# Kernel optimization log

Measured on AMD Instinct MI355X. Metric: run time of the kernel, lower is better.

Reference implementation:

```python
import jax, jax.numpy as jnp
import numpy as np

N_NODES = 50000
N_EDGES = 1600000
IN_DIM = 1024
MID_DIM = 256


def setup_inputs() -> dict:
    key = jax.random.key(0)
    k1, k2, k3, k4 = jax.random.split(key, 4)
    x = jax.random.normal(k1, (N_NODES, IN_DIM), dtype=jnp.float32)
    edge_index = jax.random.randint(k2, (2, N_EDGES), 0, N_NODES, dtype=jnp.int64)
    # Glorot-style init like PyG GCNConv
    W1 = jax.random.normal(k3, (IN_DIM, MID_DIM), dtype=jnp.float32) * (2.0 / (IN_DIM + MID_DIM)) ** 0.5
    W2 = jax.random.normal(k4, (MID_DIM, IN_DIM), dtype=jnp.float32) * (2.0 / (MID_DIM + IN_DIM)) ** 0.5
    b1 = jnp.zeros((MID_DIM,), dtype=jnp.float32)
    b2 = jnp.zeros((IN_DIM,), dtype=jnp.float32)
    return {"x": x, "edge_index": edge_index, "W1": W1, "b1": b1, "W2": W2, "b2": b2}


def _gcn_conv(x, W, b, src, dst, norm, n):
    # PyG GCNConv: linear transform first, then normalized neighbor sum, then bias.
    xw = x @ W                                   # [N, F_out]
    msg = xw[src] * norm[:, None]                # gather + scale, [E+N, F_out]
    out = jax.ops.segment_sum(msg, dst, num_segments=n)
    return out + b


def reference(x, edge_index, W1, b1, W2, b2):
    n = x.shape[0]
    loops = jnp.arange(n, dtype=edge_index.dtype)
    src = jnp.concatenate([edge_index[0], loops])
    dst = jnp.concatenate([edge_index[1], loops])
    # symmetric normalization with self-loops: D^-1/2 (A+I) D^-1/2
    deg = jax.ops.segment_sum(jnp.ones_like(dst, dtype=x.dtype), dst, num_segments=n)
    dis = jnp.where(deg > 0, jax.lax.rsqrt(jnp.maximum(deg, 1.0)), 0.0)
    norm = dis[src] * dis[dst]                   # [E+N]
    h = jax.nn.relu(_gcn_conv(x, W1, b1, src, dst, norm, n))
    # F.dropout(training=False) is identity at inference
    out = _gcn_conv(h, W2, b2, src, dst, norm, n)
    return out
```

## Files before the change

### kernel.cpp

```cpp
#include <hip/hip_runtime.h>

typedef unsigned short u16;
typedef u16 u16x8 __attribute__((ext_vector_type(8)));
typedef u16 u16x4 __attribute__((ext_vector_type(4)));
typedef short s16x8 __attribute__((ext_vector_type(8)));
typedef float f32x4 __attribute__((ext_vector_type(4)));

__device__ __forceinline__ float b2f(u16 u) {
  unsigned int v = ((unsigned int)u) << 16;
  return __builtin_bit_cast(float, v);
}
__device__ __forceinline__ u16 f2b(float f) {
  unsigned int u = __builtin_bit_cast(unsigned int, f);
  u += 0x7FFFu + ((u >> 16) & 1u);
  return (u16)(u >> 16);
}

__global__ void deg_kernel(const int* __restrict__ dst, int* __restrict__ deg, int E, int n) {
  int e = blockIdx.x * 256 + threadIdx.x;
  if (e < E) {
    int d = dst[e];
    d = min(max(d, 0), n - 1);
    atomicAdd(&deg[d], 1);
  }
}

__global__ void dis_kernel(const int* __restrict__ deg, float* __restrict__ dis, int n) {
  int i = blockIdx.x * 256 + threadIdx.x;
  if (i < n) dis[i] = 1.0f / sqrtf((float)(deg[i] + 1));
}

__global__ __launch_bounds__(256) void scanA(const int* __restrict__ cnt, int* __restrict__ bsum, int n) {
  __shared__ int s[256];
  int t = threadIdx.x, i = blockIdx.x * 256 + t;
  s[t] = (i < n) ? cnt[i] : 0;
  __syncthreads();
  for (int off = 128; off > 0; off >>= 1) {
    if (t < off) s[t] += s[t + off];
    __syncthreads();
  }
  if (t == 0) bsum[blockIdx.x] = s[0];
}

__global__ __launch_bounds__(256) void scanB(int* __restrict__ bsum, int nb) {
  __shared__ int s[256];
  int t = threadIdx.x;
  int v = (t < nb) ? bsum[t] : 0;
  s[t] = v;
  __syncthreads();
  for (int off = 1; off < 256; off <<= 1) {
    int x = (t >= off) ? s[t - off] : 0;
    __syncthreads();
    s[t] += x;
    __syncthreads();
  }
  if (t < nb) bsum[t] = s[t] - v;
}

__global__ __launch_bounds__(256) void scanC(const int* __restrict__ cnt, const int* __restrict__ bsum,
                                             int* __restrict__ rowp, int n) {
  __shared__ int s[256];
  int t = threadIdx.x, i = blockIdx.x * 256 + t;
  int v = (i < n) ? cnt[i] : 0;
  s[t] = v;
  __syncthreads();
  for (int off = 1; off < 256; off <<= 1) {
    int x = (t >= off) ? s[t - off] : 0;
    __syncthreads();
    s[t] += x;
    __syncthreads();
  }
  if (i < n) rowp[i + 1] = bsum[blockIdx.x] + s[t];
  if (i == 0) rowp[0] = 0;
}

__global__ void fill_kernel(const int* __restrict__ src, const int* __restrict__ dst,
                            const int* __restrict__ rowp, int* __restrict__ fill,
                            const float* __restrict__ dis, int* __restrict__ csr_s,
                            float* __restrict__ csr_w, int E, int n) {
  int e = blockIdx.x * 256 + threadIdx.x;
  if (e < E) {
    int s = src[e]; s = min(max(s, 0), n - 1);
    int d = dst[e]; d = min(max(d, 0), n - 1);
    int pos = rowp[d] + atomicAdd(&fill[d], 1);
    csr_s[pos] = s;
    csr_w[pos] = dis[s] * dis[d];
  }
}

__global__ void transpose_cvt(const float* __restrict__ in, u16* __restrict__ out, int K, int N) {
  int idx = blockIdx.x * 256 + threadIdx.x;
  if (idx < K * N) {
    int k = idx / N, nn = idx - k * N;
    out[(size_t)nn * K + k] = f2b(in[idx]);
  }
}

template <bool A_F32, bool OUT_F32>
__global__ __launch_bounds__(256) void gemm_kernel(const void* __restrict__ Ap,
                                                   const u16* __restrict__ BT,
                                                   const float* __restrict__ bias,
                                                   void* __restrict__ Cp, int M, int N, int K) {
  __shared__ u16 As[128 * 40];
  __shared__ u16 Bs[128 * 40];
  const int tid = threadIdx.x;
  const int m0 = blockIdx.y * 128, n0 = blockIdx.x * 128;
  const int lane = tid & 63, wv = tid >> 6;
  const int wr = (wv >> 1) * 64, wc = (wv & 1) * 64;
  const int q = lane >> 4, l = lane & 15;
  f32x4 acc[4][4] = {};

  for (int kt = 0; kt < K; kt += 32) {
    if (A_F32) {
      const float* A = (const float*)Ap;
#pragma unroll
      for (int i = 0; i < 4; i++) {
        int t = tid + i * 256;
        int r = t >> 3, k4 = (t & 7) * 4;
        float4 av = make_float4(0.f, 0.f, 0.f, 0.f);
        int gr = m0 + r;
        if (gr < M) av = *(const float4*)&A[(size_t)gr * K + kt + k4];
        u16x4 o;
        o[0] = f2b(av.x); o[1] = f2b(av.y); o[2] = f2b(av.z); o[3] = f2b(av.w);
        *(u16x4*)&As[r * 40 + k4] = o;
      }
    } else {
      const u16* A = (const u16*)Ap;
#pragma unroll
      for (int i = 0; i < 2; i++) {
        int t = tid + i * 256;
        int r = t >> 2, k8 = (t & 3) * 8;
        u16x8 av = {};
        int gr = m0 + r;
        if (gr < M) av = *(const u16x8*)&A[(size_t)gr * K + kt + k8];
        *(u16x8*)&As[r * 40 + k8] = av;
      }
    }
#pragma unroll
    for (int i = 0; i < 2; i++) {
      int t = tid + i * 256;
      int r = t >> 2, k8 = (t & 3) * 8;
      *(u16x8*)&Bs[r * 40 + k8] = *(const u16x8*)&BT[(size_t)(n0 + r) * K + kt + k8];
    }
    __syncthreads();
    s16x8 af[4], bf[4];
#pragma unroll
    for (int mi = 0; mi < 4; mi++) af[mi] = *(const s16x8*)&As[(wr + mi * 16 + l) * 40 + q * 8];
#pragma unroll
    for (int ni = 0; ni < 4; ni++) bf[ni] = *(const s16x8*)&Bs[(wc + ni * 16 + l) * 40 + q * 8];
#pragma unroll
    for (int mi = 0; mi < 4; mi++)
#pragma unroll
      for (int ni = 0; ni < 4; ni++)
        acc[mi][ni] = __builtin_amdgcn_mfma_f32_16x16x32_bf16(af[mi], bf[ni], acc[mi][ni], 0, 0, 0);
    __syncthreads();
  }

#pragma unroll
  for (int ni = 0; ni < 4; ni++) {
    int col = n0 + wc + ni * 16 + l;
    float bv = bias ? bias[col] : 0.f;
#pragma unroll
    for (int mi = 0; mi < 4; mi++) {
#pragma unroll
      for (int j = 0; j < 4; j++) {
        int row = m0 + wr + mi * 16 + q * 4 + j;
        if (row < M) {
          float v = acc[mi][ni][j] + bv;
          if (OUT_F32)
            ((float*)Cp)[(size_t)row * N + col] = v;
          else
            ((u16*)Cp)[(size_t)row * N + col] = f2b(v);
        }
      }
    }
  }
}

template <bool RELU>
__global__ __launch_bounds__(256) void agg_kernel(const u16* __restrict__ tab,
                                                  const int* __restrict__ rowp,
                                                  const int* __restrict__ csr_s,
                                                  const float* __restrict__ csr_w,
                                                  const float* __restrict__ dis,
                                                  const float* __restrict__ bias,
                                                  u16* __restrict__ out, int n) {
  int wv = threadIdx.x >> 6, lane = threadIdx.x & 63;
  int node = blockIdx.x * 4 + wv;
  if (node >= n) return;
  int f0 = lane * 4;
  float sw = dis[node];
  sw *= sw;
  u16x4 v = *(const u16x4*)&tab[(size_t)node * 256 + f0];
  float a0 = sw * b2f(v[0]), a1 = sw * b2f(v[1]), a2 = sw * b2f(v[2]), a3 = sw * b2f(v[3]);
  int e0 = rowp[node], e1 = rowp[node + 1];
  for (int e = e0; e < e1; e++) {
    int s = csr_s[e];
    float w = csr_w[e];
    u16x4 u = *(const u16x4*)&tab[(size_t)s * 256 + f0];
    a0 += w * b2f(u[0]);
    a1 += w * b2f(u[1]);
    a2 += w * b2f(u[2]);
    a3 += w * b2f(u[3]);
  }
  if (RELU) {
    a0 = fmaxf(a0 + bias[f0 + 0], 0.f);
    a1 = fmaxf(a1 + bias[f0 + 1], 0.f);
    a2 = fmaxf(a2 + bias[f0 + 2], 0.f);
    a3 = fmaxf(a3 + bias[f0 + 3], 0.f);
  }
  u16x4 o;
  o[0] = f2b(a0); o[1] = f2b(a1); o[2] = f2b(a2); o[3] = f2b(a3);
  *(u16x4*)&out[(size_t)node * 256 + f0] = o;
}

extern "C" void kernel_launch(void* const* d_in, const int* in_sizes, int n_in,
                              void* d_out, int out_size, void* d_ws, size_t ws_size,
                              hipStream_t stream) {
  const float* x  = (const float*)d_in[0];
  const int*   ei = (const int*)d_in[1];
  const float* W1 = (const float*)d_in[2];
  const float* b1 = (const float*)d_in[3];
  const float* W2 = (const float*)d_in[4];
  const float* b2 = (const float*)d_in[5];

  const int MID = in_sizes[3];
  const int IN  = in_sizes[5];
  const int n   = in_sizes[0] / IN;
  const int E   = in_sizes[1] / 2;
  const int* srcv = ei;
  const int* dstv = ei + E;

  char* w = (char*)d_ws;
  size_t off = 0;
  auto alloc = [&](size_t bytes) -> void* {
    void* p = w + off;
    off += (bytes + 255) & ~(size_t)255;
    return p;
  };
  int*   deg   = (int*)alloc((size_t)n * 4);
  int*   rowp  = (int*)alloc((size_t)(n + 1) * 4);
  int*   fill  = (int*)alloc((size_t)n * 4);
  int*   bsum  = (int*)alloc(1024);
  int*   csr_s = (int*)alloc((size_t)E * 4);
  float* csr_w = (float*)alloc((size_t)E * 4);
  float* dis   = (float*)alloc((size_t)n * 4);
  u16*   W1T   = (u16*)alloc((size_t)IN * MID * 2);
  u16*   W2T   = (u16*)alloc((size_t)IN * MID * 2);
  u16*   xw    = (u16*)alloc((size_t)n * MID * 2);
  u16*   h     = (u16*)alloc((size_t)n * MID * 2);
  u16*   ah    = xw;

  hipMemsetAsync(deg, 0, (size_t)n * 4, stream);
  hipMemsetAsync(fill, 0, (size_t)n * 4, stream);

  transpose_cvt<<<(IN * MID + 255) / 256, 256, 0, stream>>>(W1, W1T, IN, MID);
  transpose_cvt<<<(IN * MID + 255) / 256, 256, 0, stream>>>(W2, W2T, MID, IN);

  const int nb = (n + 255) / 256;
  deg_kernel<<<(E + 255) / 256, 256, 0, stream>>>(dstv, deg, E, n);
  dis_kernel<<<nb, 256, 0, stream>>>(deg, dis, n);
  scanA<<<nb, 256, 0, stream>>>(deg, bsum, n);
  scanB<<<1, 256, 0, stream>>>(bsum, nb);
  scanC<<<nb, 256, 0, stream>>>(deg, bsum, rowp, n);
  fill_kernel<<<(E + 255) / 256, 256, 0, stream>>>(srcv, dstv, rowp, fill, dis, csr_s, csr_w, E, n);

  dim3 g1(MID / 128, (n + 127) / 128);
  gemm_kernel<true, false><<<g1, 256, 0, stream>>>(x, W1T, nullptr, xw, n, MID, IN);
  agg_kernel<true><<<(n + 3) / 4, 256, 0, stream>>>(xw, rowp, csr_s, csr_w, dis, b1, h, n);
  agg_kernel<false><<<(n + 3) / 4, 256, 0, stream>>>(h, rowp, csr_s, csr_w, dis, nullptr, ah, n);
  dim3 g2(IN / 128, (n + 127) / 128);
  gemm_kernel<false, true><<<g2, 256, 0, stream>>>(ah, W2T, b2, d_out, n, IN, MID);
}
```

Measured before the change: 1.080 ms.

## Double-buffer GEMM LDS tiles and unroll edge gather loop by four

The GEMM kernel now uses two LDS buffers. It prefetches the next K-tile into registers while MFMAs run on the current tile, then stores it to the alternate buffer, so only one barrier is needed per iteration. This hides global-load latency, at the cost of double LDS use and more registers, which may lower occupancy. The aggregation kernel also unrolls its neighbor loop by four so several independent gathers are in flight at once. This changes the float summation order slightly.

```diff
diff --git a/kernel.cpp b/kernel.cpp
--- a/kernel.cpp
+++ b/kernel.cpp
@@ -101,8 +101,8 @@
                                                    const u16* __restrict__ BT,
                                                    const float* __restrict__ bias,
                                                    void* __restrict__ Cp, int M, int N, int K) {
-  __shared__ u16 As[128 * 40];
-  __shared__ u16 Bs[128 * 40];
+  __shared__ u16 As[2][128 * 40];
+  __shared__ u16 Bs[2][128 * 40];
   const int tid = threadIdx.x;
   const int m0 = blockIdx.y * 128, n0 = blockIdx.x * 128;
   const int lane = tid & 63, wv = tid >> 6;
@@ -110,19 +110,20 @@
   const int q = lane >> 4, l = lane & 15;
   f32x4 acc[4][4] = {};
 
-  for (int kt = 0; kt < K; kt += 32) {
+  float4 aregf[4];
+  u16x8 aregb[2];
+  u16x8 breg[2];
+
+  auto load_tile = [&](int kt) {
     if (A_F32) {
       const float* A = (const float*)Ap;
 #pragma unroll
       for (int i = 0; i < 4; i++) {
         int t = tid + i * 256;
         int r = t >> 3, k4 = (t & 7) * 4;
-        float4 av = make_float4(0.f, 0.f, 0.f, 0.f);
         int gr = m0 + r;
-        if (gr < M) av = *(const float4*)&A[(size_t)gr * K + kt + k4];
-        u16x4 o;
-        o[0] = f2b(av.x); o[1] = f2b(av.y); o[2] = f2b(av.z); o[3] = f2b(av.w);
-        *(u16x4*)&As[r * 40 + k4] = o;
+        aregf[i] = make_float4(0.f, 0.f, 0.f, 0.f);
+        if (gr < M) aregf[i] = *(const float4*)&A[(size_t)gr * K + kt + k4];
       }
     } else {
       const u16* A = (const u16*)Ap;
@@ -130,30 +131,69 @@
       for (int i = 0; i < 2; i++) {
         int t = tid + i * 256;
         int r = t >> 2, k8 = (t & 3) * 8;
-        u16x8 av = {};
         int gr = m0 + r;
-        if (gr < M) av = *(const u16x8*)&A[(size_t)gr * K + kt + k8];
-        *(u16x8*)&As[r * 40 + k8] = av;
+        aregb[i] = (u16x8){};
+        if (gr < M) aregb[i] = *(const u16x8*)&A[(size_t)gr * K + kt + k8];
       }
     }
 #pragma unroll
     for (int i = 0; i < 2; i++) {
       int t = tid + i * 256;
       int r = t >> 2, k8 = (t & 3) * 8;
-      *(u16x8*)&Bs[r * 40 + k8] = *(const u16x8*)&BT[(size_t)(n0 + r) * K + kt + k8];
-    }
-    __syncthreads();
+      breg[i] = *(const u16x8*)&BT[(size_t)(n0 + r) * K + kt + k8];
+    }
+  };
+
+  auto store_tile = [&](int buf) {
+    if (A_F32) {
+#pragma unroll
+      for (int i = 0; i < 4; i++) {
+        int t = tid + i * 256;
+        int r = t >> 3, k4 = (t & 7) * 4;
+        u16x4 o;
+        o[0] = f2b(aregf[i].x); o[1] = f2b(aregf[i].y);
+        o[2] = f2b(aregf[i].z); o[3] = f2b(aregf[i].w);
+        *(u16x4*)&As[buf][r * 40 + k4] = o;
+      }
+    } else {
+#pragma unroll
+      for (int i = 0; i < 2; i++) {
+        int t = tid + i * 256;
+        int r = t >> 2, k8 = (t & 3) * 8;
+        *(u16x8*)&As[buf][r * 40 + k8] = aregb[i];
+      }
+    }
+#pragma unroll
+    for (int i = 0; i < 2; i++) {
+      int t = tid + i * 256;
+      int r = t >> 2, k8 = (t & 3) * 8;
+      *(u16x8*)&Bs[buf][r * 40 + k8] = breg[i];
+    }
+  };
+
+  load_tile(0);
+  store_tile(0);
+  __syncthreads();
+
+  int cur = 0;
+  for (int kt = 0; kt < K; kt += 32) {
+    const bool has_next = (kt + 32) < K;
+    if (has_next) load_tile(kt + 32);
+
     s16x8 af[4], bf[4];
 #pragma unroll
-    for (int mi = 0; mi < 4; mi++) af[mi] = *(const s16x8*)&As[(wr + mi * 16 + l) * 40 + q * 8];
-#pragma unroll
-    for (int ni = 0; ni < 4; ni++) bf[ni] = *(const s16x8*)&Bs[(wc + ni * 16 + l) * 40 + q * 8];
+    for (int mi = 0; mi < 4; mi++) af[mi] = *(const s16x8*)&As[cur][(wr + mi * 16 + l) * 40 + q * 8];
+#pragma unroll
+    for (int ni = 0; ni < 4; ni++) bf[ni] = *(const s16x8*)&Bs[cur][(wc + ni * 16 + l) * 40 + q * 8];
 #pragma unroll
     for (int mi = 0; mi < 4; mi++)
 #pragma unroll
       for (int ni = 0; ni < 4; ni++)
         acc[mi][ni] = __builtin_amdgcn_mfma_f32_16x16x32_bf16(af[mi], bf[ni], acc[mi][ni], 0, 0, 0);
-    __syncthreads();
+
+    if (has_next) store_tile(cur ^ 1);
+    __syncthreads();
+    cur ^= 1;
   }
 
 #pragma unroll
@@ -194,7 +234,20 @@
   u16x4 v = *(const u16x4*)&tab[(size_t)node * 256 + f0];
   float a0 = sw * b2f(v[0]), a1 = sw * b2f(v[1]), a2 = sw * b2f(v[2]), a3 = sw * b2f(v[3]);
   int e0 = rowp[node], e1 = rowp[node + 1];
-  for (int e = e0; e < e1; e++) {
+  int e = e0;
+  for (; e + 4 <= e1; e += 4) {
+    int s0 = csr_s[e], s1 = csr_s[e + 1], s2 = csr_s[e + 2], s3 = csr_s[e + 3];
+    float w0 = csr_w[e], w1 = csr_w[e + 1], w2 = csr_w[e + 2], w3 = csr_w[e + 3];
+    u16x4 u0 = *(const u16x4*)&tab[(size_t)s0 * 256 + f0];
+    u16x4 u1 = *(const u16x4*)&tab[(size_t)s1 * 256 + f0];
+    u16x4 u2 = *(const u16x4*)&tab[(size_t)s2 * 256 + f0];
+    u16x4 u3 = *(const u16x4*)&tab[(size_t)s3 * 256 + f0];
+    a0 += w0 * b2f(u0[0]) + w1 * b2f(u1[0]) + w2 * b2f(u2[0]) + w3 * b2f(u3[0]);
+    a1 += w0 * b2f(u0[1]) + w1 * b2f(u1[1]) + w2 * b2f(u2[1]) + w3 * b2f(u3[1]);
+    a2 += w0 * b2f(u0[2]) + w1 * b2f(u1[2]) + w2 * b2f(u2[2]) + w3 * b2f(u3[2]);
+    a3 += w0 * b2f(u0[3]) + w1 * b2f(u1[3]) + w2 * b2f(u2[3]) + w3 * b2f(u3[3]);
+  }
+  for (; e < e1; e++) {
     int s = csr_s[e];
     float w = csr_w[e];
     u16x4 u = *(const u16x4*)&tab[(size_t)s * 256 + f0];
```

After: 878.6 us. 1.23x faster.

## Replace LDS-tiled GEMM with register-streamed double-buffered MFMA; unroll aggregation by four

Applied to the files above, without the earlier changes.

The GEMM drops shared memory and barriers. Each wave loads its A and B fragments straight from global memory into registers, double-buffered across k-steps so loads overlap MFMA work, and converts f32 to bf16 with packed cvt instructions. Tiles change to 64 rows by 256 columns per block, with each wave owning 64 columns. The aggregation loop is unrolled by four edges to keep more gathers in flight. The risks are that A and B data shared between waves is no longer reused through LDS, raising global and L2 traffic, and that register pressure grows.

```diff
diff --git a/kernel.cpp b/kernel.cpp
--- a/kernel.cpp
+++ b/kernel.cpp
@@ -97,74 +97,101 @@
 }
 
 template <bool A_F32, bool OUT_F32>
-__global__ __launch_bounds__(256) void gemm_kernel(const void* __restrict__ Ap,
+__global__ __launch_bounds__(256) void gemm_stream(const void* __restrict__ Ap,
                                                    const u16* __restrict__ BT,
                                                    const float* __restrict__ bias,
                                                    void* __restrict__ Cp, int M, int N, int K) {
-  __shared__ u16 As[128 * 40];
-  __shared__ u16 Bs[128 * 40];
   const int tid = threadIdx.x;
-  const int m0 = blockIdx.y * 128, n0 = blockIdx.x * 128;
-  const int lane = tid & 63, wv = tid >> 6;
-  const int wr = (wv >> 1) * 64, wc = (wv & 1) * 64;
-  const int q = lane >> 4, l = lane & 15;
+  const int lane = tid & 63;
+  const int wv = tid >> 6;
+  const int l = lane & 15, q = lane >> 4;
+  const int m0 = blockIdx.y * 64;
+  const int n0 = blockIdx.x * 256 + wv * 64;
+
+  const float* afp[4];
+  const u16*   abp[4];
+  const u16*   bbp[4];
+#pragma unroll
+  for (int mi = 0; mi < 4; mi++) {
+    int r = m0 + mi * 16 + l;
+    if (r > M - 1) r = M - 1;
+    if (A_F32) afp[mi] = (const float*)Ap + (size_t)r * K + q * 8;
+    else       abp[mi] = (const u16*)Ap + (size_t)r * K + q * 8;
+  }
+#pragma unroll
+  for (int ni = 0; ni < 4; ni++) {
+    int c = n0 + ni * 16 + l;
+    bbp[ni] = BT + (size_t)c * K + q * 8;
+  }
+
   f32x4 acc[4][4] = {};
-
-  for (int kt = 0; kt < K; kt += 32) {
+  float4 arA[4][2], arB[4][2];
+  u16x8 abA[4], abB[4];
+  u16x8 brA[4], brB[4];
+  s16x8 af[4];
+
+  auto loadA = [&](float4 (&ar)[4][2], u16x8 (&ab)[4], int kt) {
     if (A_F32) {
-      const float* A = (const float*)Ap;
-#pragma unroll
-      for (int i = 0; i < 4; i++) {
-        int t = tid + i * 256;
-        int r = t >> 3, k4 = (t & 7) * 4;
-        float4 av = make_float4(0.f, 0.f, 0.f, 0.f);
-        int gr = m0 + r;
-        if (gr < M) av = *(const float4*)&A[(size_t)gr * K + kt + k4];
-        u16x4 o;
-        o[0] = f2b(av.x); o[1] = f2b(av.y); o[2] = f2b(av.z); o[3] = f2b(av.w);
-        *(u16x4*)&As[r * 40 + k4] = o;
+#pragma unroll
+      for (int mi = 0; mi < 4; mi++) {
+        ar[mi][0] = *(const float4*)(afp[mi] + kt);
+        ar[mi][1] = *(const float4*)(afp[mi] + kt + 4);
       }
     } else {
-      const u16* A = (const u16*)Ap;
-#pragma unroll
-      for (int i = 0; i < 2; i++) {
-        int t = tid + i * 256;
-        int r = t >> 2, k8 = (t & 3) * 8;
-        u16x8 av = {};
-        int gr = m0 + r;
-        if (gr < M) av = *(const u16x8*)&A[(size_t)gr * K + kt + k8];
-        *(u16x8*)&As[r * 40 + k8] = av;
+#pragma unroll
+      for (int mi = 0; mi < 4; mi++) ab[mi] = *(const u16x8*)(abp[mi] + kt);
+    }
+  };
+  auto loadB = [&](u16x8 (&br)[4], int kt) {
+#pragma unroll
+    for (int ni = 0; ni < 4; ni++) br[ni] = *(const u16x8*)(bbp[ni] + kt);
+  };
+  auto cvtA = [&](float4 (&ar)[4][2], u16x8 (&ab)[4]) {
+    if (A_F32) {
+#pragma unroll
+      for (int mi = 0; mi < 4; mi++) {
+        unsigned int d0, d1, d2, d3;
+        asm("v_cvt_pk_bf16_f32 %0, %1, %2" : "=v"(d0) : "v"(ar[mi][0].x), "v"(ar[mi][0].y));
+        asm("v_cvt_pk_bf16_f32 %0, %1, %2" : "=v"(d1) : "v"(ar[mi][0].z), "v"(ar[mi][0].w));
+        asm("v_cvt_pk_bf16_f32 %0, %1, %2" : "=v"(d2) : "v"(ar[mi][1].x), "v"(ar[mi][1].y));
+        asm("v_cvt_pk_bf16_f32 %0, %1, %2" : "=v"(d3) : "v"(ar[mi][1].z), "v"(ar[mi][1].w));
+        int4 di; di.x = d0; di.y = d1; di.z = d2; di.w = d3;
+        af[mi] = __builtin_bit_cast(s16x8, di);
       }
+    } else {
+#pragma unroll
+      for (int mi = 0; mi < 4; mi++) af[mi] = __builtin_bit_cast(s16x8, ab[mi]);
     }
-#pragma unroll
-    for (int i = 0; i < 2; i++) {
-      int t = tid + i * 256;
-      int r = t >> 2, k8 = (t & 3) * 8;
-      *(u16x8*)&Bs[r * 40 + k8] = *(const u16x8*)&BT[(size_t)(n0 + r) * K + kt + k8];
-    }
-    __syncthreads();
-    s16x8 af[4], bf[4];
-#pragma unroll
-    for (int mi = 0; mi < 4; mi++) af[mi] = *(const s16x8*)&As[(wr + mi * 16 + l) * 40 + q * 8];
-#pragma unroll
-    for (int ni = 0; ni < 4; ni++) bf[ni] = *(const s16x8*)&Bs[(wc + ni * 16 + l) * 40 + q * 8];
+  };
+  auto domfma = [&](u16x8 (&br)[4]) {
 #pragma unroll
     for (int mi = 0; mi < 4; mi++)
 #pragma unroll
       for (int ni = 0; ni < 4; ni++)
-        acc[mi][ni] = __builtin_amdgcn_mfma_f32_16x16x32_bf16(af[mi], bf[ni], acc[mi][ni], 0, 0, 0);
-    __syncthreads();
+        acc[mi][ni] = __builtin_amdgcn_mfma_f32_16x16x32_bf16(
+            af[mi], __builtin_bit_cast(s16x8, br[ni]), acc[mi][ni], 0, 0, 0);
+  };
+
+  loadA(arA, abA, 0);
+  loadB(brA, 0);
+  for (int kt = 0; kt < K; kt += 64) {
+    if (kt + 32 < K) { loadA(arB, abB, kt + 32); loadB(brB, kt + 32); }
+    cvtA(arA, abA);
+    domfma(brA);
+    if (kt + 64 < K) { loadA(arA, abA, kt + 64); loadB(brA, kt + 64); }
+    cvtA(arB, abB);
+    domfma(brB);
   }
 
 #pragma unroll
   for (int ni = 0; ni < 4; ni++) {
-    int col = n0 + wc + ni * 16 + l;
+    int col = n0 + ni * 16 + l;
     float bv = bias ? bias[col] : 0.f;
 #pragma unroll
     for (int mi = 0; mi < 4; mi++) {
 #pragma unroll
       for (int j = 0; j < 4; j++) {
-        int row = m0 + wr + mi * 16 + q * 4 + j;
+        int row = m0 + mi * 16 + q * 4 + j;
         if (row < M) {
           float v = acc[mi][ni][j] + bv;
           if (OUT_F32)
@@ -194,7 +221,20 @@
   u16x4 v = *(const u16x4*)&tab[(size_t)node * 256 + f0];
   float a0 = sw * b2f(v[0]), a1 = sw * b2f(v[1]), a2 = sw * b2f(v[2]), a3 = sw * b2f(v[3]);
   int e0 = rowp[node], e1 = rowp[node + 1];
-  for (int e = e0; e < e1; e++) {
+  int e = e0;
+  for (; e + 4 <= e1; e += 4) {
+    int s0 = csr_s[e], s1 = csr_s[e + 1], s2 = csr_s[e + 2], s3 = csr_s[e + 3];
+    float w0 = csr_w[e], w1 = csr_w[e + 1], w2 = csr_w[e + 2], w3 = csr_w[e + 3];
+    u16x4 u0 = *(const u16x4*)&tab[(size_t)s0 * 256 + f0];
+    u16x4 u1 = *(const u16x4*)&tab[(size_t)s1 * 256 + f0];
+    u16x4 u2 = *(const u16x4*)&tab[(size_t)s2 * 256 + f0];
+    u16x4 u3 = *(const u16x4*)&tab[(size_t)s3 * 256 + f0];
+    a0 += w0 * b2f(u0[0]) + w1 * b2f(u1[0]) + w2 * b2f(u2[0]) + w3 * b2f(u3[0]);
+    a1 += w0 * b2f(u0[1]) + w1 * b2f(u1[1]) + w2 * b2f(u2[1]) + w3 * b2f(u3[1]);
+    a2 += w0 * b2f(u0[2]) + w1 * b2f(u1[2]) + w2 * b2f(u2[2]) + w3 * b2f(u3[2]);
+    a3 += w0 * b2f(u0[3]) + w1 * b2f(u1[3]) + w2 * b2f(u2[3]) + w3 * b2f(u3[3]);
+  }
+  for (; e < e1; e++) {
     int s = csr_s[e];
     float w = csr_w[e];
     u16x4 u = *(const u16x4*)&tab[(size_t)s * 256 + f0];
@@ -265,10 +305,10 @@
   scanC<<<nb, 256, 0, stream>>>(deg, bsum, rowp, n);
   fill_kernel<<<(E + 255) / 256, 256, 0, stream>>>(srcv, dstv, rowp, fill, dis, csr_s, csr_w, E, n);
 
-  dim3 g1(MID / 128, (n + 127) / 128);
-  gemm_kernel<true, false><<<g1, 256, 0, stream>>>(x, W1T, nullptr, xw, n, MID, IN);
+  dim3 g1(MID / 256, (n + 63) / 64);
+  gemm_stream<true, false><<<g1, 256, 0, stream>>>(x, W1T, nullptr, xw, n, MID, IN);
   agg_kernel<true><<<(n + 3) / 4, 256, 0, stream>>>(xw, rowp, csr_s, csr_w, dis, b1, h, n);
   agg_kernel<false><<<(n + 3) / 4, 256, 0, stream>>>(h, rowp, csr_s, csr_w, dis, nullptr, ah, n);
-  dim3 g2(IN / 128, (n + 127) / 128);
-  gemm_kernel<false, true><<<g2, 256, 0, stream>>>(ah, W2T, b2, d_out, n, IN, MID);
-}
+  dim3 g2(IN / 256, (n + 63) / 64);
+  gemm_stream<false, true><<<g2, 256, 0, stream>>>(ah, W2T, b2, d_out, n, IN, MID);
+}
```

Measured after the change: 974.3 us. 1.11x faster.

## Use direct global-to-LDS loads with XOR swizzle in GEMM; unroll aggregation gathers

Applied to the files above, without the earlier changes.

The GEMM tile loads now use global_load_lds to copy 16-byte chunks straight into LDS, with an XOR-swizzled layout instead of padded rows. For the fp32 input, the bf16 conversion moves to after the LDS read using v_cvt_pk_bf16_f32, so LDS holds fp32 and is twice as large. The aggregation loop is unrolled by four so several neighbour gathers are in flight at once. Together these aim to cut register staging and VGPR round trips in the loads and to raise memory-level parallelism in the gather. The out-of-range rows are now clamped rather than zeroed.

```diff
diff --git a/kernel.cpp b/kernel.cpp
--- a/kernel.cpp
+++ b/kernel.cpp
@@ -14,6 +14,12 @@
   unsigned int u = __builtin_bit_cast(unsigned int, f);
   u += 0x7FFFu + ((u >> 16) & 1u);
   return (u16)(u >> 16);
+}
+
+__device__ __forceinline__ void gld16(void* lds, const void* g) {
+  __builtin_amdgcn_global_load_lds(
+      (const __attribute__((address_space(1))) void*)g,
+      (__attribute__((address_space(3))) void*)lds, 16, 0, 0);
 }
 
 __global__ void deg_kernel(const int* __restrict__ dst, int* __restrict__ deg, int E, int n) {
@@ -97,12 +103,15 @@
 }
 
 template <bool A_F32, bool OUT_F32>
-__global__ __launch_bounds__(256) void gemm_kernel(const void* __restrict__ Ap,
-                                                   const u16* __restrict__ BT,
-                                                   const float* __restrict__ bias,
-                                                   void* __restrict__ Cp, int M, int N, int K) {
-  __shared__ u16 As[128 * 40];
-  __shared__ u16 Bs[128 * 40];
+__global__ __launch_bounds__(256) void gemm_m97(const void* __restrict__ Ap,
+                                                const u16* __restrict__ BT,
+                                                const float* __restrict__ bias,
+                                                void* __restrict__ Cp, int M, int N, int K) {
+  constexpr int ABYTES = A_F32 ? 16384 : 8192;
+  __shared__ alignas(16) unsigned char smem[ABYTES + 8192];
+  unsigned char* Asm = smem;
+  unsigned char* Bsm = smem + ABYTES;
+
   const int tid = threadIdx.x;
   const int m0 = blockIdx.y * 128, n0 = blockIdx.x * 128;
   const int lane = tid & 63, wv = tid >> 6;
@@ -110,44 +119,76 @@
   const int q = lane >> 4, l = lane & 15;
   f32x4 acc[4][4] = {};
 
+  constexpr int NA = A_F32 ? 4 : 2;
+  constexpr size_t AB = A_F32 ? 4 : 2;
+  const char* a_src[NA];
+  const char* b_src[2];
+#pragma unroll
+  for (int i = 0; i < NA; i++) {
+    int c = tid + i * 256;
+    int r, lb;
+    if (A_F32) {
+      r = c >> 3;
+      int sb = (c & 7) * 16;
+      lb = sb ^ ((r & 7) << 4);
+    } else {
+      r = c >> 2;
+      int sb = (c & 3) * 16;
+      lb = sb ^ ((r & 3) << 4);
+    }
+    int gr = m0 + r;
+    if (gr > M - 1) gr = M - 1;
+    a_src[i] = (const char*)Ap + (size_t)gr * K * AB + lb;
+  }
+#pragma unroll
+  for (int i = 0; i < 2; i++) {
+    int c = tid + i * 256;
+    int r = c >> 2;
+    int sb = (c & 3) * 16;
+    int lb = sb ^ ((r & 3) << 4);
+    b_src[i] = (const char*)BT + (size_t)(n0 + r) * K * 2 + lb;
+  }
+
   for (int kt = 0; kt < K; kt += 32) {
+#pragma unroll
+    for (int i = 0; i < NA; i++)
+      gld16(Asm + (tid + i * 256) * 16, a_src[i] + (size_t)kt * AB);
+#pragma unroll
+    for (int i = 0; i < 2; i++)
+      gld16(Bsm + (tid + i * 256) * 16, b_src[i] + (size_t)kt * 2);
+    __syncthreads();
+
+    s16x8 af[4], bf[4];
     if (A_F32) {
-      const float* A = (const float*)Ap;
-#pragma unroll
-      for (int i = 0; i < 4; i++) {
-        int t = tid + i * 256;
-        int r = t >> 3, k4 = (t & 7) * 4;
-        float4 av = make_float4(0.f, 0.f, 0.f, 0.f);
-        int gr = m0 + r;
-        if (gr < M) av = *(const float4*)&A[(size_t)gr * K + kt + k4];
-        u16x4 o;
-        o[0] = f2b(av.x); o[1] = f2b(av.y); o[2] = f2b(av.z); o[3] = f2b(av.w);
-        *(u16x4*)&As[r * 40 + k4] = o;
+#pragma unroll
+      for (int mi = 0; mi < 4; mi++) {
+        int R = wr + mi * 16 + l;
+        int xr = (R & 7) << 4;
+        const char* rb = (const char*)Asm + R * 128;
+        float4 lo = *(const float4*)(rb + ((q * 32) ^ xr));
+        float4 hi = *(const float4*)(rb + ((q * 32 + 16) ^ xr));
+        unsigned int d0, d1, d2, d3;
+        asm("v_cvt_pk_bf16_f32 %0, %1, %2" : "=v"(d0) : "v"(lo.x), "v"(lo.y));
+        asm("v_cvt_pk_bf16_f32 %0, %1, %2" : "=v"(d1) : "v"(lo.z), "v"(lo.w));
+        asm("v_cvt_pk_bf16_f32 %0, %1, %2" : "=v"(d2) : "v"(hi.x), "v"(hi.y));
+        asm("v_cvt_pk_bf16_f32 %0, %1, %2" : "=v"(d3) : "v"(hi.z), "v"(hi.w));
+        int4 di;
+        di.x = (int)d0; di.y = (int)d1; di.z = (int)d2; di.w = (int)d3;
+        af[mi] = __builtin_bit_cast(s16x8, di);
       }
     } else {
-      const u16* A = (const u16*)Ap;
-#pragma unroll
-      for (int i = 0; i < 2; i++) {
-        int t = tid + i * 256;
-        int r = t >> 2, k8 = (t & 3) * 8;
-        u16x8 av = {};
-        int gr = m0 + r;
-        if (gr < M) av = *(const u16x8*)&A[(size_t)gr * K + kt + k8];
-        *(u16x8*)&As[r * 40 + k8] = av;
+#pragma unroll
+      for (int mi = 0; mi < 4; mi++) {
+        int R = wr + mi * 16 + l;
+        af[mi] = *(const s16x8*)((const char*)Asm + R * 64 + ((q * 16) ^ ((R & 3) << 4)));
       }
     }
 #pragma unroll
-    for (int i = 0; i < 2; i++) {
-      int t = tid + i * 256;
-      int r = t >> 2, k8 = (t & 3) * 8;
-      *(u16x8*)&Bs[r * 40 + k8] = *(const u16x8*)&BT[(size_t)(n0 + r) * K + kt + k8];
+    for (int ni = 0; ni < 4; ni++) {
+      int C = wc + ni * 16 + l;
+      bf[ni] = *(const s16x8*)((const char*)Bsm + C * 64 + ((q * 16) ^ ((C & 3) << 4)));
     }
-    __syncthreads();
-    s16x8 af[4], bf[4];
-#pragma unroll
-    for (int mi = 0; mi < 4; mi++) af[mi] = *(const s16x8*)&As[(wr + mi * 16 + l) * 40 + q * 8];
-#pragma unroll
-    for (int ni = 0; ni < 4; ni++) bf[ni] = *(const s16x8*)&Bs[(wc + ni * 16 + l) * 40 + q * 8];
+
 #pragma unroll
     for (int mi = 0; mi < 4; mi++)
 #pragma unroll
@@ -194,7 +235,20 @@
   u16x4 v = *(const u16x4*)&tab[(size_t)node * 256 + f0];
   float a0 = sw * b2f(v[0]), a1 = sw * b2f(v[1]), a2 = sw * b2f(v[2]), a3 = sw * b2f(v[3]);
   int e0 = rowp[node], e1 = rowp[node + 1];
-  for (int e = e0; e < e1; e++) {
+  int e = e0;
+  for (; e + 4 <= e1; e += 4) {
+    int s0 = csr_s[e], s1 = csr_s[e + 1], s2 = csr_s[e + 2], s3 = csr_s[e + 3];
+    float w0 = csr_w[e], w1 = csr_w[e + 1], w2 = csr_w[e + 2], w3 = csr_w[e + 3];
+    u16x4 u0 = *(const u16x4*)&tab[(size_t)s0 * 256 + f0];
+    u16x4 u1 = *(const u16x4*)&tab[(size_t)s1 * 256 + f0];
+    u16x4 u2 = *(const u16x4*)&tab[(size_t)s2 * 256 + f0];
+    u16x4 u3 = *(const u16x4*)&tab[(size_t)s3 * 256 + f0];
+    a0 += w0 * b2f(u0[0]) + w1 * b2f(u1[0]) + w2 * b2f(u2[0]) + w3 * b2f(u3[0]);
+    a1 += w0 * b2f(u0[1]) + w1 * b2f(u1[1]) + w2 * b2f(u2[1]) + w3 * b2f(u3[1]);
+    a2 += w0 * b2f(u0[2]) + w1 * b2f(u1[2]) + w2 * b2f(u2[2]) + w3 * b2f(u3[2]);
+    a3 += w0 * b2f(u0[3]) + w1 * b2f(u1[3]) + w2 * b2f(u2[3]) + w3 * b2f(u3[3]);
+  }
+  for (; e < e1; e++) {
     int s = csr_s[e];
     float w = csr_w[e];
     u16x4 u = *(const u16x4*)&tab[(size_t)s * 256 + f0];
@@ -266,9 +320,9 @@
   fill_kernel<<<(E + 255) / 256, 256, 0, stream>>>(srcv, dstv, rowp, fill, dis, csr_s, csr_w, E, n);
 
   dim3 g1(MID / 128, (n + 127) / 128);
-  gemm_kernel<true, false><<<g1, 256, 0, stream>>>(x, W1T, nullptr, xw, n, MID, IN);
+  gemm_m97<true, false><<<g1, 256, 0, stream>>>(x, W1T, nullptr, xw, n, MID, IN);
   agg_kernel<true><<<(n + 3) / 4, 256, 0, stream>>>(xw, rowp, csr_s, csr_w, dis, b1, h, n);
   agg_kernel<false><<<(n + 3) / 4, 256, 0, stream>>>(h, rowp, csr_s, csr_w, dis, nullptr, ah, n);
   dim3 g2(IN / 128, (n + 127) / 128);
-  gemm_kernel<false, true><<<g2, 256, 0, stream>>>(ah, W2T, b2, d_out, n, IN, MID);
-}
+  gemm_m97<false, true><<<g2, 256, 0, stream>>>(ah, W2T, b2, d_out, n, IN, MID);
+}
```

Result: faster. 891.2 us (-17.5%).
